# Performance work log

Hardware: AMD Instinct MI355X
Metric: run time of the kernel (lower is better)

Reference implementation:

```python
import jax, jax.numpy as jnp
import numpy as np

M = 100000   # BS*L nodes
D_IN = 256   # in_d
D_OUT = 256  # out_d
E = 1024     # number of edges; indices index the out_d axis (faithful to source quirk)


def setup_inputs() -> dict:
    key = jax.random.key(0)
    k1, k2, k3 = jax.random.split(key, 3)
    node_features = jax.random.normal(k1, (1, M, D_IN), dtype=jnp.float32)
    W = jax.random.normal(k2, (D_OUT, D_IN), dtype=jnp.float32) * (1.0 / np.sqrt(D_IN))
    b = jnp.zeros((D_OUT,), dtype=jnp.float32)
    edge_mapping = jax.random.randint(k3, (2, E), 0, D_OUT, dtype=jnp.int64)
    batch_lens = jnp.ones((M, 1), dtype=jnp.float32)
    return {"node_features": node_features, "W": W, "b": b,
            "edge_mapping": edge_mapping, "batch_lens": batch_lens}


def reference(node_features, W, b, edge_mapping, batch_lens):
    # fc: [1, M, in_d] -> [1, M, out_d]
    h = jnp.einsum('bmi,oi->bmo', node_features, W) + b
    residual = h                              # [1, M, D_OUT]
    hf = jnp.swapaxes(h, 1, 2)[0]             # [D_OUT, M]  (transpose(2,1).squeeze(0))
    gathered = hf[edge_mapping[1]]            # [E, M]      (index_select dim=0)
    agg = jnp.zeros_like(hf).at[edge_mapping[0]].add(gathered)  # scatter-add, [D_OUT, M]
    new_nf = agg.T                            # [M, D_OUT]
    out = (new_nf + residual) / batch_lens    # broadcast -> [1, M, D_OUT]
    return out
```

## Files before the change

kernel.cpp:

```cpp
#include <hip/hip_runtime.h>
#include <cstdint>

constexpr int D = 256;

typedef __bf16 bf16x8 __attribute__((ext_vector_type(8)));
typedef float  f32x4  __attribute__((ext_vector_type(4)));

__global__ void prep_copy(const float* __restrict__ W, const float* __restrict__ b,
                          float* __restrict__ W2, float* __restrict__ b2) {
    int i = blockIdx.x * 256 + threadIdx.x;
    W2[i] = W[i];
    if (blockIdx.x == 0) b2[threadIdx.x] = b[threadIdx.x];
}

__global__ void prep_edges(const int* __restrict__ em, int E,
                           const float* __restrict__ W, const float* __restrict__ b,
                           float* __restrict__ W2, float* __restrict__ b2) {
    int e = blockIdx.x;
    int k = threadIdx.x;
    int dst = em[e];
    int src = em[E + e];
    atomicAdd(&W2[dst * D + k], W[src * D + k]);
    if (k == 0) atomicAdd(&b2[dst], b[src]);
}

__global__ void prep_convert(const float* __restrict__ W2, ushort* __restrict__ Wh) {
    int i = blockIdx.x * 256 + threadIdx.x;
    int o = i >> 8, k = i & 255;
    uint32_t u = __float_as_uint(W2[i]);
    uint32_t r = u + 0x7FFFu + ((u >> 16) & 1u);
    int kc = k >> 5, kk = k & 31, q = kk >> 3, j = kk & 7;
    int idx = kc * 8192 + (((o >> 4) * 4 + q) * 16 + (o & 15)) * 8 + j;
    Wh[idx] = (ushort)(r >> 16);
}

__device__ __forceinline__ void cvt8(const float4& f0, const float4& f1,
                                     bf16x8& hi8, bf16x8& lo8) {
    float xs[8] = {f0.x, f0.y, f0.z, f0.w, f1.x, f1.y, f1.z, f1.w};
    uint32_t h[8], l[8];
    #pragma unroll
    for (int j = 0; j < 8; ++j) {
        uint32_t u  = __float_as_uint(xs[j]);
        uint32_t hu = u & 0xFFFF0000u;
        h[j] = hu;
        float r = xs[j] - __uint_as_float(hu);
        uint32_t ru = __float_as_uint(r);
        l[j] = ru + 0x7FFFu + ((ru >> 16) & 1u);
    }
    uint4 hp = make_uint4((h[0] >> 16) | (h[1] & 0xFFFF0000u),
                          (h[2] >> 16) | (h[3] & 0xFFFF0000u),
                          (h[4] >> 16) | (h[5] & 0xFFFF0000u),
                          (h[6] >> 16) | (h[7] & 0xFFFF0000u));
    uint4 lp = make_uint4((l[0] >> 16) | (l[1] & 0xFFFF0000u),
                          (l[2] >> 16) | (l[3] & 0xFFFF0000u),
                          (l[4] >> 16) | (l[5] & 0xFFFF0000u),
                          (l[6] >> 16) | (l[7] & 0xFFFF0000u));
    hi8 = *(bf16x8*)&hp;
    lo8 = *(bf16x8*)&lp;
}

__global__ __launch_bounds__(256) void resgcn_mfma(
    const float* __restrict__ X, const ushort* __restrict__ Whg,
    const float* __restrict__ b2, const float* __restrict__ blen,
    float* __restrict__ out, int M)
{
    const int tid  = threadIdx.x;
    const int lane = tid & 63;
    const int w    = tid >> 6;
    const int wm   = w >> 1;
    const int wo   = w & 1;
    const int bid  = blockIdx.x;
    const int ob   = bid & 1;
    const int mb   = bid >> 1;

    const int m0 = mb * 128 + wm * 64;
    const int ob16 = ob * 8 + wo * 4;

    const float* pA[4];
    #pragma unroll
    for (int a = 0; a < 4; ++a) {
        int r = m0 + a * 16 + (lane & 15);
        if (r >= M) r = M - 1;
        pA[a] = X + (size_t)r * D + ((lane >> 4) * 8);
    }
    const ushort* pB = Whg + ((size_t)ob16 * 64 + lane) * 8;

    f32x4 acc[4][4];
    #pragma unroll
    for (int a = 0; a < 4; ++a)
        #pragma unroll
        for (int b = 0; b < 4; ++b) acc[a][b] = (f32x4){0.f, 0.f, 0.f, 0.f};

    float4 xa[4][2];
    bf16x8 bf[4];
    #pragma unroll
    for (int a = 0; a < 4; ++a) {
        xa[a][0] = *(const float4*)(pA[a]);
        xa[a][1] = *(const float4*)(pA[a] + 4);
    }
    #pragma unroll
    for (int b = 0; b < 4; ++b) bf[b] = *(const bf16x8*)(pB + b * 512);

    for (int kc = 0; kc < 8; ++kc) {
        float4 nxa[4][2];
        bf16x8 nbf[4];
        if (kc < 7) {
            #pragma unroll
            for (int a = 0; a < 4; ++a) {
                const float* p = pA[a] + (kc + 1) * 32;
                nxa[a][0] = *(const float4*)(p);
                nxa[a][1] = *(const float4*)(p + 4);
            }
            const ushort* q = pB + (size_t)(kc + 1) * 8192;
            #pragma unroll
            for (int b = 0; b < 4; ++b) nbf[b] = *(const bf16x8*)(q + b * 512);
        }

        bf16x8 ah[4], al[4];
        #pragma unroll
        for (int a = 0; a < 4; ++a) cvt8(xa[a][0], xa[a][1], ah[a], al[a]);

        #pragma unroll
        for (int a = 0; a < 4; ++a)
            #pragma unroll
            for (int b = 0; b < 4; ++b) {
                acc[a][b] = __builtin_amdgcn_mfma_f32_16x16x32_bf16(ah[a], bf[b], acc[a][b], 0, 0, 0);
                acc[a][b] = __builtin_amdgcn_mfma_f32_16x16x32_bf16(al[a], bf[b], acc[a][b], 0, 0, 0);
            }

        if (kc < 7) {
            #pragma unroll
            for (int a = 0; a < 4; ++a) { xa[a][0] = nxa[a][0]; xa[a][1] = nxa[a][1]; }
            #pragma unroll
            for (int b = 0; b < 4; ++b) bf[b] = nbf[b];
        }
    }

    const int col = lane & 15;
    const int rq  = lane >> 4;
    float bias[4];
    #pragma unroll
    for (int b = 0; b < 4; ++b) bias[b] = b2[(ob16 + b) * 16 + col];

    #pragma unroll
    for (int a = 0; a < 4; ++a) {
        #pragma unroll
        for (int r = 0; r < 4; ++r) {
            int m = m0 + a * 16 + rq * 4 + r;
            if (m < M) {
                float inv = 1.0f / blen[m];
                #pragma unroll
                for (int b = 0; b < 4; ++b) {
                    int o = (ob16 + b) * 16 + col;
                    out[(size_t)m * D + o] = (acc[a][b][r] + bias[b]) * inv;
                }
            }
        }
    }
}

extern "C" void kernel_launch(void* const* d_in, const int* in_sizes, int n_in,
                              void* d_out, int out_size, void* d_ws, size_t ws_size,
                              hipStream_t stream) {
    (void)n_in; (void)out_size; (void)ws_size;
    const float* X  = (const float*)d_in[0];
    const float* W  = (const float*)d_in[1];
    const float* b  = (const float*)d_in[2];
    const int*   em = (const int*)d_in[3];
    const float* bl = (const float*)d_in[4];
    float* out = (float*)d_out;

    const int M = in_sizes[0] / D;
    const int E = in_sizes[3] / 2;

    float*  W2 = (float*)d_ws;
    float*  b2 = W2 + D * D;
    ushort* Wh = (ushort*)(b2 + D);

    prep_copy<<<D * D / 256, 256, 0, stream>>>(W, b, W2, b2);
    prep_edges<<<E, D, 0, stream>>>(em, E, W, b, W2, b2);
    prep_convert<<<D * D / 256, 256, 0, stream>>>(W2, Wh);

    int mblocks = (M + 127) / 128;
    resgcn_mfma<<<mblocks * 2, 256, 0, stream>>>(X, Wh, b2, bl, out, M);
}
```

Before: 232.3 us.

## Switch to 32x32x16 MFMA tiles with deeper X prefetch and perm-based bf16 split

```diff
diff --git a/kernel.cpp b/kernel.cpp
--- a/kernel.cpp
+++ b/kernel.cpp
@@ -3,8 +3,8 @@
 
 constexpr int D = 256;
 
-typedef __bf16 bf16x8 __attribute__((ext_vector_type(8)));
-typedef float  f32x4  __attribute__((ext_vector_type(4)));
+typedef __bf16 bf16x8  __attribute__((ext_vector_type(8)));
+typedef float  f32x16  __attribute__((ext_vector_type(16)));
 
 __global__ void prep_copy(const float* __restrict__ W, const float* __restrict__ b,
                           float* __restrict__ W2, float* __restrict__ b2) {
@@ -29,34 +29,31 @@
     int o = i >> 8, k = i & 255;
     uint32_t u = __float_as_uint(W2[i]);
     uint32_t r = u + 0x7FFFu + ((u >> 16) & 1u);
-    int kc = k >> 5, kk = k & 31, q = kk >> 3, j = kk & 7;
-    int idx = kc * 8192 + (((o >> 4) * 4 + q) * 16 + (o & 15)) * 8 + j;
+    int ks = k >> 4, kh = (k >> 3) & 1, j = k & 7;
+    int lane = (o & 31) + 32 * kh;
+    int idx = ((ks * 8 + (o >> 5)) * 64 + lane) * 8 + j;
     Wh[idx] = (ushort)(r >> 16);
 }
 
-__device__ __forceinline__ void cvt8(const float4& f0, const float4& f1,
-                                     bf16x8& hi8, bf16x8& lo8) {
+__device__ __forceinline__ void cvt8p(const float4& f0, const float4& f1,
+                                      bf16x8& hi8, bf16x8& lo8) {
     float xs[8] = {f0.x, f0.y, f0.z, f0.w, f1.x, f1.y, f1.z, f1.w};
-    uint32_t h[8], l[8];
+    uint32_t hp[4], lp[4];
     #pragma unroll
-    for (int j = 0; j < 8; ++j) {
-        uint32_t u  = __float_as_uint(xs[j]);
-        uint32_t hu = u & 0xFFFF0000u;
-        h[j] = hu;
-        float r = xs[j] - __uint_as_float(hu);
-        uint32_t ru = __float_as_uint(r);
-        l[j] = ru + 0x7FFFu + ((ru >> 16) & 1u);
+    for (int j = 0; j < 4; ++j) {
+        uint32_t u0 = __float_as_uint(xs[2 * j]);
+        uint32_t u1 = __float_as_uint(xs[2 * j + 1]);
+        uint32_t h0 = u0 & 0xFFFF0000u;
+        uint32_t h1 = u1 & 0xFFFF0000u;
+        float r0 = xs[2 * j]     - __uint_as_float(h0);
+        float r1 = xs[2 * j + 1] - __uint_as_float(h1);
+        hp[j] = __builtin_amdgcn_perm(h1, h0, 0x07060302u);
+        lp[j] = __builtin_amdgcn_perm(__float_as_uint(r1), __float_as_uint(r0), 0x07060302u);
     }
-    uint4 hp = make_uint4((h[0] >> 16) | (h[1] & 0xFFFF0000u),
-                          (h[2] >> 16) | (h[3] & 0xFFFF0000u),
-                          (h[4] >> 16) | (h[5] & 0xFFFF0000u),
-                          (h[6] >> 16) | (h[7] & 0xFFFF0000u));
-    uint4 lp = make_uint4((l[0] >> 16) | (l[1] & 0xFFFF0000u),
-                          (l[2] >> 16) | (l[3] & 0xFFFF0000u),
-                          (l[4] >> 16) | (l[5] & 0xFFFF0000u),
-                          (l[6] >> 16) | (l[7] & 0xFFFF0000u));
-    hi8 = *(bf16x8*)&hp;
-    lo8 = *(bf16x8*)&lp;
+    uint4 h4 = make_uint4(hp[0], hp[1], hp[2], hp[3]);
+    uint4 l4 = make_uint4(lp[0], lp[1], lp[2], lp[3]);
+    hi8 = *(bf16x8*)&h4;
+    lo8 = *(bf16x8*)&l4;
 }
 
 __global__ __launch_bounds__(256) void resgcn_mfma(
@@ -67,94 +64,82 @@
     const int tid  = threadIdx.x;
     const int lane = tid & 63;
     const int w    = tid >> 6;
-    const int wm   = w >> 1;
-    const int wo   = w & 1;
     const int bid  = blockIdx.x;
-    const int ob   = bid & 1;
-    const int mb   = bid >> 1;
+    const int oc   = bid & 3;
+    const int mb   = bid >> 2;
 
-    const int m0 = mb * 128 + wm * 64;
-    const int ob16 = ob * 8 + wo * 4;
+    const int m0 = mb * 128 + w * 32;
+    int row = m0 + (lane & 31);
+    if (row >= M) row = M - 1;
+    const int kh = lane >> 5;
+    const float* xp = X + (size_t)row * D + kh * 8;
 
-    const float* pA[4];
+    const ushort* bp = Whg + (size_t)(oc * 2) * 512 + lane * 8;
+
+    f32x16 acc[2];
+    acc[0] = (f32x16)(0.f);
+    acc[1] = (f32x16)(0.f);
+
+    float4 xb[3][4];
+    bf16x8 bb[2][4];
+
+    #define LOAD_X(kc, slot)                                                  \
+        { const float* p = xp + (kc) * 32;                                    \
+          xb[slot][0] = *(const float4*)(p);                                  \
+          xb[slot][1] = *(const float4*)(p + 4);                              \
+          xb[slot][2] = *(const float4*)(p + 16);                             \
+          xb[slot][3] = *(const float4*)(p + 20); }
+    #define LOAD_B(kc, slot)                                                  \
+        { const ushort* q = bp + (size_t)(kc) * 2 * 8 * 512;                  \
+          bb[slot][0] = *(const bf16x8*)(q);                                  \
+          bb[slot][1] = *(const bf16x8*)(q + 512);                            \
+          bb[slot][2] = *(const bf16x8*)(q + 8 * 512);                        \
+          bb[slot][3] = *(const bf16x8*)(q + 9 * 512); }
+
+    LOAD_X(0, 0)
+    LOAD_X(1, 1)
+    LOAD_B(0, 0)
+
     #pragma unroll
-    for (int a = 0; a < 4; ++a) {
-        int r = m0 + a * 16 + (lane & 15);
-        if (r >= M) r = M - 1;
-        pA[a] = X + (size_t)r * D + ((lane >> 4) * 8);
+    for (int kc = 0; kc < 8; ++kc) {
+        const int cur3 = kc % 3;
+        const int cur2 = kc & 1;
+        if (kc + 2 < 8) LOAD_X(kc + 2, (kc + 2) % 3)
+        if (kc + 1 < 8) LOAD_B(kc + 1, (kc + 1) & 1)
+
+        bf16x8 ah[2], al[2];
+        cvt8p(xb[cur3][0], xb[cur3][1], ah[0], al[0]);
+        cvt8p(xb[cur3][2], xb[cur3][3], ah[1], al[1]);
+
+        #pragma unroll
+        for (int s = 0; s < 2; ++s)
+            #pragma unroll
+            for (int ob = 0; ob < 2; ++ob) {
+                acc[ob] = __builtin_amdgcn_mfma_f32_32x32x16_bf16(
+                              ah[s], bb[cur2][s * 2 + ob], acc[ob], 0, 0, 0);
+                acc[ob] = __builtin_amdgcn_mfma_f32_32x32x16_bf16(
+                              al[s], bb[cur2][s * 2 + ob], acc[ob], 0, 0, 0);
+            }
     }
-    const ushort* pB = Whg + ((size_t)ob16 * 64 + lane) * 8;
+    #undef LOAD_X
+    #undef LOAD_B
 
-    f32x4 acc[4][4];
+    const int col = lane & 31;
+    float inv16[16];
     #pragma unroll
-    for (int a = 0; a < 4; ++a)
-        #pragma unroll
-        for (int b = 0; b < 4; ++b) acc[a][b] = (f32x4){0.f, 0.f, 0.f, 0.f};
-
-    float4 xa[4][2];
-    bf16x8 bf[4];
-    #pragma unroll
-    for (int a = 0; a < 4; ++a) {
-        xa[a][0] = *(const float4*)(pA[a]);
-        xa[a][1] = *(const float4*)(pA[a] + 4);
+    for (int r = 0; r < 16; ++r) {
+        int m = m0 + (r & 3) + 8 * (r >> 2) + 4 * kh;
+        inv16[r] = 1.0f / blen[(m < M) ? m : (M - 1)];
     }
     #pragma unroll
-    for (int b = 0; b < 4; ++b) bf[b] = *(const bf16x8*)(pB + b * 512);
-
-    for (int kc = 0; kc < 8; ++kc) {
-        float4 nxa[4][2];
-        bf16x8 nbf[4];
-        if (kc < 7) {
-            #pragma unroll
-            for (int a = 0; a < 4; ++a) {
-                const float* p = pA[a] + (kc + 1) * 32;
-                nxa[a][0] = *(const float4*)(p);
-                nxa[a][1] = *(const float4*)(p + 4);
-            }
-            const ushort* q = pB + (size_t)(kc + 1) * 8192;
-            #pragma unroll
-            for (int b = 0; b < 4; ++b) nbf[b] = *(const bf16x8*)(q + b * 512);
-        }
-
-        bf16x8 ah[4], al[4];
+    for (int ob = 0; ob < 2; ++ob) {
+        int o = oc * 64 + ob * 32 + col;
+        float bias = b2[o];
         #pragma unroll
-        for (int a = 0; a < 4; ++a) cvt8(xa[a][0], xa[a][1], ah[a], al[a]);
-
-        #pragma unroll
-        for (int a = 0; a < 4; ++a)
-            #pragma unroll
-            for (int b = 0; b < 4; ++b) {
-                acc[a][b] = __builtin_amdgcn_mfma_f32_16x16x32_bf16(ah[a], bf[b], acc[a][b], 0, 0, 0);
-                acc[a][b] = __builtin_amdgcn_mfma_f32_16x16x32_bf16(al[a], bf[b], acc[a][b], 0, 0, 0);
-            }
-
-        if (kc < 7) {
-            #pragma unroll
-            for (int a = 0; a < 4; ++a) { xa[a][0] = nxa[a][0]; xa[a][1] = nxa[a][1]; }
-            #pragma unroll
-            for (int b = 0; b < 4; ++b) bf[b] = nbf[b];
-        }
-    }
-
-    const int col = lane & 15;
-    const int rq  = lane >> 4;
-    float bias[4];
-    #pragma unroll
-    for (int b = 0; b < 4; ++b) bias[b] = b2[(ob16 + b) * 16 + col];
-
-    #pragma unroll
-    for (int a = 0; a < 4; ++a) {
-        #pragma unroll
-        for (int r = 0; r < 4; ++r) {
-            int m = m0 + a * 16 + rq * 4 + r;
-            if (m < M) {
-                float inv = 1.0f / blen[m];
-                #pragma unroll
-                for (int b = 0; b < 4; ++b) {
-                    int o = (ob16 + b) * 16 + col;
-                    out[(size_t)m * D + o] = (acc[a][b][r] + bias[b]) * inv;
-                }
-            }
+        for (int r = 0; r < 16; ++r) {
+            int m = m0 + (r & 3) + 8 * (r >> 2) + 4 * kh;
+            if (m < M)
+                out[(size_t)m * D + o] = (acc[ob][r] + bias) * inv16[r];
         }
     }
 }
@@ -182,5 +167,5 @@
     prep_convert<<<D * D / 256, 256, 0, stream>>>(W2, Wh);
 
     int mblocks = (M + 127) / 128;
-    resgcn_mfma<<<mblocks * 2, 256, 0, stream>>>(X, Wh, b2, bl, out, M);
+    resgcn_mfma<<<mblocks * 4, 256, 0, stream>>>(X, Wh, b2, bl, out, M);
 }
```

Measured after the change: 255.3 us. 1.1x slower.
